# Kernel optimization log

Hardware: AMD Instinct MI355X
Metric: run time of the kernel (lower is better)

## Reference

```python
import math
import jax, jax.numpy as jnp
import numpy as np

LMAX = 10
R_REF = 6371000.0
N = 1_000_000


def _sh_renorm(l, m, fourpi=True):
    base = math.sqrt((2.0 * l + 1.0) * math.factorial(l - abs(m)) / (4.0 * math.pi * math.factorial(l + abs(m))))
    if fourpi:
        base *= math.sqrt(4.0 * math.pi)
    return base


def _assoc_legendre(l, m, x):
    # P_l^m(x) via the standard stable recursion; l, m are Python ints (unrolled at trace time).
    pmm = jnp.ones_like(x)
    if m > 0:
        somx2 = jnp.sqrt(jnp.clip((1.0 - x) * (1.0 + x), 0.0, None))
        fact = 1.0
        for _ in range(1, m + 1):
            pmm = pmm * (-fact) * somx2
            fact += 2.0
    if l == m:
        return pmm
    pmmp1 = x * (2.0 * m + 1.0) * pmm
    if l == m + 1:
        return pmmp1
    pll = pmmp1
    for ll in range(m + 2, l + 1):
        pll = ((2.0 * ll - 1.0) * x * pmmp1 - (ll + m - 1.0) * pmm) / (ll - m)
        pmm = pmmp1
        pmmp1 = pll
    return pll


def _sh(m, l, phi, theta):
    cos_theta = jnp.clip(jnp.cos(theta), -1.0 + 1e-07, 1.0 - 1e-07)
    P_lm = _assoc_legendre(l, abs(m), cos_theta)
    K_lm = _sh_renorm(l, m)
    if m == 0:
        return K_lm * P_lm
    elif m > 0:
        return math.sqrt(2.0) * K_lm * jnp.cos(m * phi) * P_lm
    else:
        return math.sqrt(2.0) * K_lm * jnp.sin(-m * phi) * P_lm


def setup_inputs() -> dict:
    key = jax.random.key(0)
    k1, k2, k3 = jax.random.split(key, 3)
    lon = jax.random.uniform(k1, (N,), jnp.float32, -180.0, 180.0)
    lat = jax.random.uniform(k2, (N,), jnp.float32, -89.0, 89.0)
    r = R_REF * (1.0 + 0.01 * jax.random.uniform(k3, (N,), jnp.float32))
    return {"lonlatr": jnp.stack([lon, lat, r], axis=-1)}


def reference(lonlatr):
    lon, lat, r = lonlatr[:, 0], lonlatr[:, 1], lonlatr[:, 2]
    phi = jnp.deg2rad(lon + 180.0)
    theta = jnp.clip(jnp.deg2rad(90.0 - lat), 1e-07, math.pi - 1e-07)
    Y = []
    for l in range(LMAX + 1):
        for m in range(-l, l + 1):
            Y.append(_sh(m, l, phi, theta))
    Y = jnp.stack(Y, axis=-1)  # (N, (LMAX+1)^2)
    deg_idx = jnp.asarray(np.repeat(np.arange(LMAX + 1), 2 * np.arange(LMAX + 1) + 1), dtype=jnp.float32)
    radial_factor = (R_REF / r)[:, None] ** deg_idx[None, :]
    return Y * radial_factor
```

## Files before the change

kernel.cpp:

```cpp
#include <hip/hip_runtime.h>
#include <hip/hip_fp16.h>
#include <math.h>

#define LMAX 10
#define NCOL 121
#define PPB  64
#define TILEH (PPB * NCOL)
#define TILE4 (PPB * NCOL / 4)

typedef float f4_t __attribute__((ext_vector_type(4)));

struct Tab {
    float K[66];
    float A[66];
    float B[66];
};

template<int M, typename ST, typename EMIT>
__device__ __forceinline__ void chain(const Tab& t, ST* __restrict__ row,
                                      float pmm, float rfm, float rf, float x,
                                      float cm, float sm, EMIT emit) {
    {
        float v = t.K[M * (M + 1) / 2 + M] * pmm * rfm;
        if constexpr (M == 0) emit(row, 0, v);
        else { emit(row, M * M + 2 * M, v * cm); emit(row, M * M, v * sm); }
    }
    if constexpr (M < LMAX) {
        float p0 = pmm;
        float p1 = x * (float)(2 * M + 1) * pmm;
        float rfl = rfm * rf;
        {
            constexpr int L = M + 1;
            float v = t.K[L * (L + 1) / 2 + M] * p1 * rfl;
            if constexpr (M == 0) emit(row, L * L + L, v);
            else { emit(row, L * L + L + M, v * cm); emit(row, L * L + L - M, v * sm); }
        }
#pragma unroll
        for (int ll = M + 2; ll <= LMAX; ++ll) {
            int ti = ll * (ll + 1) / 2 + M;
            float p2 = t.A[ti] * x * p1 - t.B[ti] * p0;
            p0 = p1; p1 = p2;
            rfl *= rf;
            float v = t.K[ti] * p1 * rfl;
            int jb = ll * ll + ll;
            if constexpr (M == 0) emit(row, jb, v);
            else { emit(row, jb + M, v * cm); emit(row, jb - M, v * sm); }
        }
    }
}

template<typename ST, typename EMIT>
__device__ __forceinline__ void compute_tile(const float* __restrict__ in,
                                             long long gp, int s, const Tab& t,
                                             ST* __restrict__ row, EMIT emit) {
    const float lon = in[gp * 3 + 0];
    const float lat = in[gp * 3 + 1];
    const float r   = in[gp * 3 + 2];

    const float D2R  = 0.017453292519943295f;
    const float PI_F = 3.14159265358979323846f;

    float phi   = (lon + 180.0f) * D2R;
    float theta = fminf(fmaxf((90.0f - lat) * D2R, 1e-7f), PI_F - 1e-7f);
    float x = __cosf(theta);
    x = fminf(fmaxf(x, -1.0f + 1e-7f), 1.0f - 1e-7f);
    float somx2 = sqrtf(fmaxf((1.0f - x) * (1.0f + x), 0.0f));
    float rf  = 6371000.0f / r;
    float rf2 = rf * rf;
    float rf3 = rf2 * rf;
    float rf5 = rf3 * rf2;

    float c1, s1;
    __sincosf(phi, &s1, &c1);
    float c2 = c1 * c1 - s1 * s1, s2 = 2.0f * c1 * s1;
    float c3 = c2 * c1 - s2 * s1, s3 = s2 * c1 + c2 * s1;
    float c5 = (c2 * c2 - s2 * s2) * c1 - 2.0f * c2 * s2 * s1;
    float s5 = 2.0f * c2 * s2 * c1 + (c2 * c2 - s2 * s2) * s1;

    float sx2 = somx2 * somx2;
    float sx3 = sx2 * somx2;
    float sx5 = sx3 * sx2;

#define ROT(cm, sm, ck, sk) { float cn = cm * ck - sm * sk; sm = sm * ck + cm * sk; cm = cn; }
    switch (s) {
    case 0: {
        float pmm = 1.0f, rfm = 1.0f, cm = 1.0f, sm = 0.0f;
        chain<0>(t, row, pmm, rfm, rf, x, cm, sm, emit);
        pmm *= -945.0f    * sx5; rfm *= rf5; ROT(cm, sm, c5, s5);
        chain<5>(t, row, pmm, rfm, rf, x, cm, sm, emit);
        pmm *= -692835.0f * sx5; rfm *= rf5; ROT(cm, sm, c5, s5);
        chain<10>(t, row, pmm, rfm, rf, x, cm, sm, emit);
    } break;
    case 1: {
        float pmm = -somx2, rfm = rf, cm = c1, sm = s1;
        chain<1>(t, row, pmm, rfm, rf, x, cm, sm, emit);
        pmm *= -10395.0f * sx5; rfm *= rf5; ROT(cm, sm, c5, s5);
        chain<6>(t, row, pmm, rfm, rf, x, cm, sm, emit);
        pmm *= -3315.0f  * sx3; rfm *= rf3; ROT(cm, sm, c3, s3);
        chain<9>(t, row, pmm, rfm, rf, x, cm, sm, emit);
    } break;
    case 2: {
        float pmm = 3.0f * sx2, rfm = rf2, cm = c2, sm = s2;
        chain<2>(t, row, pmm, rfm, rf, x, cm, sm, emit);
        pmm *= -45045.0f * sx5; rfm *= rf5; ROT(cm, sm, c5, s5);
        chain<7>(t, row, pmm, rfm, rf, x, cm, sm, emit);
        pmm *= -15.0f * somx2;  rfm *= rf;  ROT(cm, sm, c1, s1);
        chain<8>(t, row, pmm, rfm, rf, x, cm, sm, emit);
    } break;
    default: {
        float pmm = -15.0f * sx3, rfm = rf3, cm = c3, sm = s3;
        chain<3>(t, row, pmm, rfm, rf, x, cm, sm, emit);
        pmm *= -7.0f * somx2; rfm *= rf; ROT(cm, sm, c1, s1);
        chain<4>(t, row, pmm, rfm, rf, x, cm, sm, emit);
    } break;
    }
#undef ROT
}

struct EmitH {
    __device__ void operator()(__half* row, int j, float v) const {
        row[j] = __float2half(v);
    }
};
struct EmitF {
    __device__ void operator()(float* row, int j, float v) const {
        row[j] = v;
    }
};

__global__ __launch_bounds__(256, 8)
void sh_main(const float* __restrict__ in, float* __restrict__ out, Tab t) {
    __shared__ __half lds[TILEH];

    const int p = threadIdx.x & 63;
    const int s = threadIdx.x >> 6;

    compute_tile(in, (long long)blockIdx.x * PPB + p, s, t,
                 &lds[p * NCOL], EmitH{});
    __syncthreads();

    f4_t* __restrict__ dst = (f4_t*)out + (long long)blockIdx.x * TILE4;
    const uint2* __restrict__ src = (const uint2*)lds;
#pragma unroll
    for (int k = 0; k < 7; ++k) {
        int i = threadIdx.x + k * 256;
        uint2 h = src[i];
        float2 fa = __half22float2(*(const __half2*)&h.x);
        float2 fb = __half22float2(*(const __half2*)&h.y);
        f4_t v = {fa.x, fa.y, fb.x, fb.y};
        __builtin_nontemporal_store(v, &dst[i]);
    }
    if (threadIdx.x < TILE4 - 7 * 256) {
        int i = threadIdx.x + 7 * 256;
        uint2 h = src[i];
        float2 fa = __half22float2(*(const __half2*)&h.x);
        float2 fb = __half22float2(*(const __half2*)&h.y);
        f4_t v = {fa.x, fa.y, fb.x, fb.y};
        __builtin_nontemporal_store(v, &dst[i]);
    }
}

__global__ __launch_bounds__(256)
void sh_tail(const float* __restrict__ in, float* __restrict__ out,
             int n, int tile0, Tab t) {
    __shared__ float lds[PPB * NCOL];
    const int p = threadIdx.x & 63;
    const int s = threadIdx.x >> 6;
    const long long gp = (long long)tile0 * PPB + p;
    if (gp < n)
        compute_tile(in, gp, s, t, &lds[p * NCOL], EmitF{});
    __syncthreads();
    const long long lim4 = ((long long)n * NCOL + 3) / 4;
    const long long base4 = (long long)tile0 * TILE4;
    f4_t* dst = (f4_t*)out + base4;
    const f4_t* src = (const f4_t*)lds;
    for (int f = threadIdx.x; f < TILE4; f += 256)
        if (base4 + f < lim4)
            __builtin_nontemporal_store(src[f], &dst[f]);
}

extern "C" void kernel_launch(void* const* d_in, const int* in_sizes, int n_in,
                              void* d_out, int out_size, void* d_ws, size_t ws_size,
                              hipStream_t stream) {
    const float* in = (const float*)d_in[0];
    float* out = (float*)d_out;
    const int n = in_sizes[0] / 3;

    Tab t;
    double fact[2 * LMAX + 1];
    fact[0] = 1.0;
    for (int i = 1; i <= 2 * LMAX; ++i) fact[i] = fact[i - 1] * (double)i;
    for (int l = 0; l <= LMAX; ++l) {
        for (int m = 0; m <= l; ++m) {
            int ti = l * (l + 1) / 2 + m;
            double k = sqrt((2.0 * l + 1.0) * fact[l - m] / fact[l + m]);
            if (m > 0) k *= sqrt(2.0);
            t.K[ti] = (float)k;
            if (l >= m + 2) {
                t.A[ti] = (float)((2.0 * l - 1.0) / (double)(l - m));
                t.B[ti] = (float)(((double)(l + m) - 1.0) / (double)(l - m));
            } else {
                t.A[ti] = 0.0f; t.B[ti] = 0.0f;
            }
        }
    }

    const int full_tiles = n / PPB;
    if (full_tiles > 0)
        sh_main<<<full_tiles, 256, 0, stream>>>(in, out, t);
    if (n - full_tiles * PPB > 0)
        sh_tail<<<1, 256, 0, stream>>>(in, out, n, full_tiles, t);
}
```

Before: 97.65 us.

## Give each wavefront a full point tile and drop block-wide barrier

Each 64-lane wavefront now computes every spherical-harmonic column for its own 64-point tile, instead of four wavefronts sharing one tile by splitting the m-sets. The LDS tile becomes per-wave, so the __syncthreads is replaced by a local lgkmcnt wait and each wave writes its own tile independently. This removes the block barrier and repeats the per-point setup only once per point, but each thread now does four times the chain work serially. The shared-memory footprint per block grows fourfold, which may cut occupancy.

```diff
diff --git a/kernel.cpp b/kernel.cpp
--- a/kernel.cpp
+++ b/kernel.cpp
@@ -5,6 +5,7 @@
 #define LMAX 10
 #define NCOL 121
 #define PPB  64
+#define WPB  4
 #define TILEH (PPB * NCOL)
 #define TILE4 (PPB * NCOL / 4)
 
@@ -49,10 +50,16 @@
     }
 }
 
-template<typename ST, typename EMIT>
-__device__ __forceinline__ void compute_tile(const float* __restrict__ in,
-                                             long long gp, int s, const Tab& t,
-                                             ST* __restrict__ row, EMIT emit) {
+#define ROT(cm, sm, ck, sk) { float cn = cm * ck - sm * sk; sm = sm * ck + cm * sk; cm = cn; }
+
+struct Setup {
+    float x, somx2, rf, rf2, rf3, rf5;
+    float c1, s1, c2, s2, c3, s3, c5, s5;
+    float sx2, sx3, sx5;
+};
+
+__device__ __forceinline__ Setup sh_setup(const float* __restrict__ in, long long gp) {
+    Setup u;
     const float lon = in[gp * 3 + 0];
     const float lat = in[gp * 3 + 1];
     const float r   = in[gp * 3 + 2];
@@ -64,57 +71,69 @@
     float theta = fminf(fmaxf((90.0f - lat) * D2R, 1e-7f), PI_F - 1e-7f);
     float x = __cosf(theta);
     x = fminf(fmaxf(x, -1.0f + 1e-7f), 1.0f - 1e-7f);
-    float somx2 = sqrtf(fmaxf((1.0f - x) * (1.0f + x), 0.0f));
-    float rf  = 6371000.0f / r;
-    float rf2 = rf * rf;
-    float rf3 = rf2 * rf;
-    float rf5 = rf3 * rf2;
-
-    float c1, s1;
-    __sincosf(phi, &s1, &c1);
-    float c2 = c1 * c1 - s1 * s1, s2 = 2.0f * c1 * s1;
-    float c3 = c2 * c1 - s2 * s1, s3 = s2 * c1 + c2 * s1;
-    float c5 = (c2 * c2 - s2 * s2) * c1 - 2.0f * c2 * s2 * s1;
-    float s5 = 2.0f * c2 * s2 * c1 + (c2 * c2 - s2 * s2) * s1;
-
-    float sx2 = somx2 * somx2;
-    float sx3 = sx2 * somx2;
-    float sx5 = sx3 * sx2;
-
-#define ROT(cm, sm, ck, sk) { float cn = cm * ck - sm * sk; sm = sm * ck + cm * sk; cm = cn; }
+    u.x = x;
+    u.somx2 = sqrtf(fmaxf((1.0f - x) * (1.0f + x), 0.0f));
+    u.rf  = 6371000.0f / r;
+    u.rf2 = u.rf * u.rf;
+    u.rf3 = u.rf2 * u.rf;
+    u.rf5 = u.rf3 * u.rf2;
+
+    __sincosf(phi, &u.s1, &u.c1);
+    u.c2 = u.c1 * u.c1 - u.s1 * u.s1;  u.s2 = 2.0f * u.c1 * u.s1;
+    u.c3 = u.c2 * u.c1 - u.s2 * u.s1;  u.s3 = u.s2 * u.c1 + u.c2 * u.s1;
+    float c4 = u.c2 * u.c2 - u.s2 * u.s2, s4 = 2.0f * u.c2 * u.s2;
+    u.c5 = c4 * u.c1 - s4 * u.s1;      u.s5 = s4 * u.c1 + c4 * u.s1;
+
+    u.sx2 = u.somx2 * u.somx2;
+    u.sx3 = u.sx2 * u.somx2;
+    u.sx5 = u.sx3 * u.sx2;
+    return u;
+}
+
+template<typename ST, typename EMIT>
+__device__ __forceinline__ void compute_mset(const Setup& u, int s, const Tab& t,
+                                             ST* __restrict__ row, EMIT emit) {
     switch (s) {
     case 0: {
         float pmm = 1.0f, rfm = 1.0f, cm = 1.0f, sm = 0.0f;
-        chain<0>(t, row, pmm, rfm, rf, x, cm, sm, emit);
-        pmm *= -945.0f    * sx5; rfm *= rf5; ROT(cm, sm, c5, s5);
-        chain<5>(t, row, pmm, rfm, rf, x, cm, sm, emit);
-        pmm *= -692835.0f * sx5; rfm *= rf5; ROT(cm, sm, c5, s5);
-        chain<10>(t, row, pmm, rfm, rf, x, cm, sm, emit);
+        chain<0>(t, row, pmm, rfm, u.rf, u.x, cm, sm, emit);
+        pmm *= -945.0f    * u.sx5; rfm *= u.rf5; ROT(cm, sm, u.c5, u.s5);
+        chain<5>(t, row, pmm, rfm, u.rf, u.x, cm, sm, emit);
+        pmm *= -692835.0f * u.sx5; rfm *= u.rf5; ROT(cm, sm, u.c5, u.s5);
+        chain<10>(t, row, pmm, rfm, u.rf, u.x, cm, sm, emit);
     } break;
     case 1: {
-        float pmm = -somx2, rfm = rf, cm = c1, sm = s1;
-        chain<1>(t, row, pmm, rfm, rf, x, cm, sm, emit);
-        pmm *= -10395.0f * sx5; rfm *= rf5; ROT(cm, sm, c5, s5);
-        chain<6>(t, row, pmm, rfm, rf, x, cm, sm, emit);
-        pmm *= -3315.0f  * sx3; rfm *= rf3; ROT(cm, sm, c3, s3);
-        chain<9>(t, row, pmm, rfm, rf, x, cm, sm, emit);
+        float pmm = -u.somx2, rfm = u.rf, cm = u.c1, sm = u.s1;
+        chain<1>(t, row, pmm, rfm, u.rf, u.x, cm, sm, emit);
+        pmm *= -10395.0f * u.sx5; rfm *= u.rf5; ROT(cm, sm, u.c5, u.s5);
+        chain<6>(t, row, pmm, rfm, u.rf, u.x, cm, sm, emit);
+        pmm *= -3315.0f  * u.sx3; rfm *= u.rf3; ROT(cm, sm, u.c3, u.s3);
+        chain<9>(t, row, pmm, rfm, u.rf, u.x, cm, sm, emit);
     } break;
     case 2: {
-        float pmm = 3.0f * sx2, rfm = rf2, cm = c2, sm = s2;
-        chain<2>(t, row, pmm, rfm, rf, x, cm, sm, emit);
-        pmm *= -45045.0f * sx5; rfm *= rf5; ROT(cm, sm, c5, s5);
-        chain<7>(t, row, pmm, rfm, rf, x, cm, sm, emit);
-        pmm *= -15.0f * somx2;  rfm *= rf;  ROT(cm, sm, c1, s1);
-        chain<8>(t, row, pmm, rfm, rf, x, cm, sm, emit);
+        float pmm = 3.0f * u.sx2, rfm = u.rf2, cm = u.c2, sm = u.s2;
+        chain<2>(t, row, pmm, rfm, u.rf, u.x, cm, sm, emit);
+        pmm *= -45045.0f * u.sx5; rfm *= u.rf5; ROT(cm, sm, u.c5, u.s5);
+        chain<7>(t, row, pmm, rfm, u.rf, u.x, cm, sm, emit);
+        pmm *= -15.0f * u.somx2;  rfm *= u.rf;  ROT(cm, sm, u.c1, u.s1);
+        chain<8>(t, row, pmm, rfm, u.rf, u.x, cm, sm, emit);
     } break;
     default: {
-        float pmm = -15.0f * sx3, rfm = rf3, cm = c3, sm = s3;
-        chain<3>(t, row, pmm, rfm, rf, x, cm, sm, emit);
-        pmm *= -7.0f * somx2; rfm *= rf; ROT(cm, sm, c1, s1);
-        chain<4>(t, row, pmm, rfm, rf, x, cm, sm, emit);
-    } break;
-    }
-#undef ROT
+        float pmm = -15.0f * u.sx3, rfm = u.rf3, cm = u.c3, sm = u.s3;
+        chain<3>(t, row, pmm, rfm, u.rf, u.x, cm, sm, emit);
+        pmm *= -7.0f * u.somx2; rfm *= u.rf; ROT(cm, sm, u.c1, u.s1);
+        chain<4>(t, row, pmm, rfm, u.rf, u.x, cm, sm, emit);
+    } break;
+    }
+}
+
+template<typename ST, typename EMIT>
+__device__ __forceinline__ void compute_point_all(const Setup& u, const Tab& t,
+                                                  ST* __restrict__ row, EMIT emit) {
+    compute_mset(u, 0, t, row, emit);
+    compute_mset(u, 1, t, row, emit);
+    compute_mset(u, 2, t, row, emit);
+    compute_mset(u, 3, t, row, emit);
 }
 
 struct EmitH {
@@ -128,30 +147,35 @@
     }
 };
 
-__global__ __launch_bounds__(256, 8)
-void sh_main(const float* __restrict__ in, float* __restrict__ out, Tab t) {
-    __shared__ __half lds[TILEH];
-
-    const int p = threadIdx.x & 63;
-    const int s = threadIdx.x >> 6;
-
-    compute_tile(in, (long long)blockIdx.x * PPB + p, s, t,
-                 &lds[p * NCOL], EmitH{});
-    __syncthreads();
-
-    f4_t* __restrict__ dst = (f4_t*)out + (long long)blockIdx.x * TILE4;
-    const uint2* __restrict__ src = (const uint2*)lds;
+__global__ __launch_bounds__(256)
+void sh_main(const float* __restrict__ in, float* __restrict__ out,
+             int ntiles, Tab t) {
+    __shared__ __half lds[WPB][TILEH];
+
+    const int w    = threadIdx.x >> 6;
+    const int lane = threadIdx.x & 63;
+    const int wtile = blockIdx.x * WPB + w;
+    if (wtile >= ntiles) return;
+
+    __half* row = &lds[w][lane * NCOL];
+    Setup u = sh_setup(in, (long long)wtile * PPB + lane);
+    compute_point_all(u, t, row, EmitH{});
+
+    asm volatile("s_waitcnt lgkmcnt(0)" ::: "memory");
+
+    const uint2* __restrict__ src = (const uint2*)&lds[w][0];
+    f4_t* __restrict__ dst = (f4_t*)out + (long long)wtile * TILE4;
 #pragma unroll
-    for (int k = 0; k < 7; ++k) {
-        int i = threadIdx.x + k * 256;
+    for (int k = 0; k < 30; ++k) {
+        int i = lane + k * 64;
         uint2 h = src[i];
         float2 fa = __half22float2(*(const __half2*)&h.x);
         float2 fb = __half22float2(*(const __half2*)&h.y);
         f4_t v = {fa.x, fa.y, fb.x, fb.y};
         __builtin_nontemporal_store(v, &dst[i]);
     }
-    if (threadIdx.x < TILE4 - 7 * 256) {
-        int i = threadIdx.x + 7 * 256;
+    if (lane < 16) {
+        int i = lane + 30 * 64;
         uint2 h = src[i];
         float2 fa = __half22float2(*(const __half2*)&h.x);
         float2 fb = __half22float2(*(const __half2*)&h.y);
@@ -167,8 +191,10 @@
     const int p = threadIdx.x & 63;
     const int s = threadIdx.x >> 6;
     const long long gp = (long long)tile0 * PPB + p;
-    if (gp < n)
-        compute_tile(in, gp, s, t, &lds[p * NCOL], EmitF{});
+    if (gp < n) {
+        Setup u = sh_setup(in, gp);
+        compute_mset(u, s, t, &lds[p * NCOL], EmitF{});
+    }
     __syncthreads();
     const long long lim4 = ((long long)n * NCOL + 3) / 4;
     const long long base4 = (long long)tile0 * TILE4;
@@ -206,8 +232,10 @@
     }
 
     const int full_tiles = n / PPB;
-    if (full_tiles > 0)
-        sh_main<<<full_tiles, 256, 0, stream>>>(in, out, t);
+    if (full_tiles > 0) {
+        const int blocks = (full_tiles + WPB - 1) / WPB;
+        sh_main<<<blocks, 256, 0, stream>>>(in, out, full_tiles, t);
+    }
     if (n - full_tiles * PPB > 0)
         sh_tail<<<1, 256, 0, stream>>>(in, out, n, full_tiles, t);
 }
```

Result: faster. 93.37 us, median of 2 (-4.4%).
